# Kernel optimization log

Hardware: AMD Instinct MI355X
Metric: run time of the kernel (lower is better)

The kernel has to match this reference:

```python
import jax, jax.numpy as jnp
import numpy as np

EMBED_DIM = 1024
NUM_HEAD = 16
HEAD_DIM = EMBED_DIM // NUM_HEAD
SCALE = HEAD_DIM ** -0.5


def setup_inputs() -> dict:
    key = jax.random.key(0)
    ks = jax.random.split(key, 8)
    B, N, K, D = 2, 2048, 2048, EMBED_DIM
    s = D ** -0.5
    return {
        "x": jax.random.normal(ks[0], (B, N, D), jnp.float32),
        "ctx": jax.random.normal(ks[1], (B, K, D), jnp.float32),
        "Wq": jax.random.normal(ks[2], (D, D), jnp.float32) * s,
        "bq": jnp.zeros((D,), jnp.float32),
        "Wkv": jax.random.normal(ks[3], (D, 2 * D), jnp.float32) * s,
        "bkv": jnp.zeros((2 * D,), jnp.float32),
        "Wproj": jax.random.normal(ks[4], (D, D), jnp.float32) * s,
        "bproj": jnp.zeros((D,), jnp.float32),
    }


def reference(x, ctx, Wq, bq, Wkv, bkv, Wproj, bproj):
    B, N, D = x.shape
    K = ctx.shape[1]
    H, hd = NUM_HEAD, HEAD_DIM
    # Q projection -> [B, H, N, hd]
    q = (x @ Wq + bq).reshape(B, N, H, hd).transpose(0, 2, 1, 3)
    # KV projection -> k, v each [B, H, K, hd]
    kv = (ctx @ Wkv + bkv).reshape(B, K, 2, H, hd).transpose(2, 0, 3, 1, 4)
    k, v = kv[0], kv[1]
    # scaled dot-product attention with materialized scores [B, H, N, K]
    attn = jnp.einsum("bhnd,bhkd->bhnk", q * SCALE, k)
    attn = jax.nn.softmax(attn, axis=-1)
    out = jnp.einsum("bhnk,bhkd->bhnd", attn, v)
    out = out.transpose(0, 2, 1, 3).reshape(B, N, D)
    return out @ Wproj + bproj
```

## Files before the change

kernel.cpp:

```cpp
#include <hip/hip_runtime.h>
#include <hip/hip_bf16.h>

typedef __attribute__((ext_vector_type(8))) short bf16x8;
typedef __attribute__((ext_vector_type(4))) float f32x4;
typedef __attribute__((ext_vector_type(16))) float f32x16;
typedef unsigned short u16;
typedef unsigned int u32;

#define NUM_HEAD 16
#define HEAD_DIM 64
#define SEQ_N 2048
#define SEQ_K 2048
#define EMB 1024
#define MROWS 4096
static constexpr float ATTN_SCALE_LOG2E = 0.125f * 1.44269504f;

#if __has_builtin(__builtin_amdgcn_exp2f)
#define EXP2(x) __builtin_amdgcn_exp2f(x)
#else
#define EXP2(x) __expf(0.69314718056f * (x))
#endif

__device__ __forceinline__ u16 f2bf(float f) {
  __hip_bfloat16 h = __float2bfloat16(f);
  return *reinterpret_cast<u16*>(&h);
}

__device__ __forceinline__ u32 pack2(float lo, float hi) {
  __hip_bfloat162 h = __float22bfloat162_rn(make_float2(lo, hi));
  return *reinterpret_cast<u32*>(&h);
}

__device__ __forceinline__ void plswap(u32& a, u32& b) {
  auto r = __builtin_amdgcn_permlane32_swap(a, b, false, false);
  a = r[0]; b = r[1];
}

__device__ __forceinline__ void async16(const u16* g, u16* l) {
  __builtin_amdgcn_global_load_lds(
      (const __attribute__((address_space(1))) unsigned int*)g,
      (__attribute__((address_space(3))) unsigned int*)l, 16, 0, 0);
}

__global__ __launch_bounds__(256) void cvt2(const float* __restrict__ x,
                                            const float* __restrict__ ctx,
                                            u16* __restrict__ xb, u16* __restrict__ cb) {
  const int n4 = MROWS * EMB / 4;
  int gid = blockIdx.x * 256 + threadIdx.x;
  const float4* s; ushort4* d; int i;
  if (gid < n4) { s = (const float4*)x;   d = (ushort4*)xb; i = gid; }
  else          { s = (const float4*)ctx; d = (ushort4*)cb; i = gid - n4; }
  float4 v = s[i];
  ushort4 o;
  o.x = f2bf(v.x); o.y = f2bf(v.y); o.z = f2bf(v.z); o.w = f2bf(v.w);
  d[i] = o;
}

__global__ __launch_bounds__(256) void transpose_cvt4(
    const float* __restrict__ Wq, const float* __restrict__ Wkv,
    const float* __restrict__ Wproj,
    u16* __restrict__ Wqt, u16* __restrict__ Wkvt, u16* __restrict__ Wpt) {
  __shared__ float tile[32][33];
  const int z = blockIdx.z;
  const float* W; u16* Wt; int srcN, colbase;
  if (z == 0)      { W = Wq;    Wt = Wqt;                          srcN = 1024; colbase = 0; }
  else if (z == 1) { W = Wkv;   Wt = Wkvt;                         srcN = 2048; colbase = 0; }
  else if (z == 2) { W = Wkv;   Wt = Wkvt + (size_t)1024 * 1024;   srcN = 2048; colbase = 1024; }
  else             { W = Wproj; Wt = Wpt;                          srcN = 1024; colbase = 0; }
  int n0 = blockIdx.x * 32, k0 = blockIdx.y * 32;
  int tx = threadIdx.x & 31, ty = threadIdx.x >> 5;
  #pragma unroll
  for (int i = ty; i < 32; i += 8)
    tile[i][tx] = W[(size_t)(k0 + i) * srcN + colbase + n0 + tx];
  __syncthreads();
  #pragma unroll
  for (int i = ty; i < 32; i += 8)
    Wt[(size_t)(n0 + i) * 1024 + k0 + tx] = f2bf(tile[tx][i]);
}

__global__ __launch_bounds__(256, 3) void gemm_qkv(
    const u16* __restrict__ xb, const u16* __restrict__ cb,
    const u16* __restrict__ Wqt, const u16* __restrict__ Wkvt,
    const float* __restrict__ bq, const float* __restrict__ bkv,
    u16* __restrict__ Qb, u16* __restrict__ Kb, u16* __restrict__ Vtb)
{
  __shared__ alignas(16) u16 smem[(128 + 128) * 64];
  u16* As = smem;
  u16* Bs = smem + 128 * 64;
  const int tid = threadIdx.x;
  const bool isQ = (blockIdx.y < 8);
  const int n0 = (isQ ? blockIdx.y : blockIdx.y - 8) * 128;
  const int m0 = blockIdx.x * 128;
  const u16* A      = isQ ? xb : cb;
  const u16* Wt     = isQ ? Wqt : Wkvt;
  const float* bias = isQ ? bq : bkv;
  const int wave = tid >> 6, lane = tid & 63;
  const int wm = (wave >> 1) * 64, wn = (wave & 1) * 64;
  const int l15 = lane & 15, quad = lane >> 4;

  f32x4 acc[4][4];
  #pragma unroll
  for (int i = 0; i < 4; i++)
    #pragma unroll
    for (int j = 0; j < 4; j++)
      #pragma unroll
      for (int r = 0; r < 4; r++) acc[i][j][r] = 0.0f;

  const int srow = tid >> 3;
  const int scol = (tid & 7) * 8;
  const u16* ag = A + (size_t)(m0 + srow) * EMB + scol;
  const u16* bg = Wt + (size_t)(n0 + srow) * EMB + scol;
  const int ldsoff = tid * 8;

  for (int kt = 0; kt < EMB; kt += 64) {
    #pragma unroll
    for (int s = 0; s < 4; s++) {
      async16(ag + (size_t)(s * 32) * EMB + kt, &As[ldsoff + s * 2048]);
      async16(bg + (size_t)(s * 32) * EMB + kt, &Bs[ldsoff + s * 2048]);
    }
    __syncthreads();
    #pragma unroll
    for (int ks = 0; ks < 2; ks++) {
      bf16x8 af[4], bfr[4];
      #pragma unroll
      for (int i = 0; i < 4; i++)
        af[i]  = *(const bf16x8*)&As[(wm + i * 16 + l15) * 64 + ks * 32 + quad * 8];
      #pragma unroll
      for (int j = 0; j < 4; j++)
        bfr[j] = *(const bf16x8*)&Bs[(wn + j * 16 + l15) * 64 + ks * 32 + quad * 8];
      #pragma unroll
      for (int i = 0; i < 4; i++)
        #pragma unroll
        for (int j = 0; j < 4; j++)
          acc[i][j] = __builtin_amdgcn_mfma_f32_16x16x32_bf16(af[i], bfr[j], acc[i][j], 0, 0, 0);
    }
    __syncthreads();
  }

  const int h = ((n0 + wn) >> 6) & 15;
  if (isQ) {
    #pragma unroll
    for (int j = 0; j < 4; j++) {
      const int gc = n0 + wn + j * 16 + l15;
      const float bv = bias[gc];
      const int d = j * 16 + l15;
      #pragma unroll
      for (int i = 0; i < 4; i++) {
        #pragma unroll
        for (int r = 0; r < 4; r++) {
          const int gm = m0 + wm + i * 16 + quad * 4 + r;
          const int bb = gm >> 11, nn = gm & 2047;
          Qb[((size_t)(bb * NUM_HEAD + h) * SEQ_N + nn) * HEAD_DIM + d] =
              f2bf((acc[i][j][r] + bv) * ATTN_SCALE_LOG2E);
        }
      }
    }
  } else if ((n0 >> 10) == 0) {
    #pragma unroll
    for (int j = 0; j < 4; j++) {
      const int gc = n0 + wn + j * 16 + l15;
      const float bv = bias[gc];
      const int d = j * 16 + l15;
      #pragma unroll
      for (int i = 0; i < 4; i++) {
        #pragma unroll
        for (int r = 0; r < 4; r++) {
          const int gm = m0 + wm + i * 16 + quad * 4 + r;
          const int bb = gm >> 11, kk = gm & 2047;
          Kb[((size_t)(bb * NUM_HEAD + h) * SEQ_K + kk) * HEAD_DIM + d] =
              f2bf(acc[i][j][r] + bv);
        }
      }
    }
  } else {
    u16* wbuf = smem + wave * 1088;
    const int gm0 = m0 + wm;
    const int bb = gm0 >> 11;
    const int kk0 = gm0 & 2047;
    #pragma unroll
    for (int j = 0; j < 4; j++) {
      const int gc = n0 + wn + j * 16 + l15;
      const float bv = bias[gc];
      #pragma unroll
      for (int i = 0; i < 4; i++) {
        ushort4 pk;
        pk.x = f2bf(acc[i][j][0] + bv);
        pk.y = f2bf(acc[i][j][1] + bv);
        pk.z = f2bf(acc[i][j][2] + bv);
        pk.w = f2bf(acc[i][j][3] + bv);
        *(ushort4*)&wbuf[l15 * 68 + i * 16 + quad * 4] = pk;
      }
      #pragma unroll
      for (int it = 0; it < 2; it++) {
        const int dd = it * 8 + (lane >> 3);
        const int kp = (lane & 7) * 8;
        uint4 v = *(const uint4*)&wbuf[dd * 68 + kp];
        *(uint4*)(Vtb + ((size_t)(bb * NUM_HEAD + h) * HEAD_DIM + j * 16 + dd) * SEQ_K
                  + kk0 + kp) = v;
      }
    }
  }
}

__global__ __launch_bounds__(256) void gemm_proj(
    const u16* __restrict__ A, const u16* __restrict__ Wt,
    const float* __restrict__ bias, float* __restrict__ outF)
{
  __shared__ alignas(16) u16 smem[(64 + 128) * 64];
  u16* As = smem;
  u16* Bs = smem + 64 * 64;
  const int tid = threadIdx.x;
  const int n0 = blockIdx.y * 128, m0 = blockIdx.x * 64;
  const int wave = tid >> 6, lane = tid & 63;
  const int wm = (wave >> 1) * 32, wn = (wave & 1) * 64;
  const int l15 = lane & 15, quad = lane >> 4;

  f32x4 acc[2][4];
  #pragma unroll
  for (int i = 0; i < 2; i++)
    #pragma unroll
    for (int j = 0; j < 4; j++)
      #pragma unroll
      for (int r = 0; r < 4; r++) acc[i][j][r] = 0.0f;

  const int srow = tid >> 3;
  const int scol = (tid & 7) * 8;
  const u16* ag = A + (size_t)(m0 + srow) * EMB + scol;
  const u16* bg = Wt + (size_t)(n0 + srow) * EMB + scol;
  const int ldsoff = tid * 8;

  for (int kt = 0; kt < EMB; kt += 64) {
    async16(ag + kt, &As[ldsoff]);
    async16(ag + (size_t)32 * EMB + kt, &As[ldsoff + 2048]);
    #pragma unroll
    for (int s = 0; s < 4; s++)
      async16(bg + (size_t)(s * 32) * EMB + kt, &Bs[ldsoff + s * 2048]);
    __syncthreads();
    #pragma unroll
    for (int ks = 0; ks < 2; ks++) {
      bf16x8 af[2], bfr[4];
      #pragma unroll
      for (int i = 0; i < 2; i++)
        af[i]  = *(const bf16x8*)&As[(wm + i * 16 + l15) * 64 + ks * 32 + quad * 8];
      #pragma unroll
      for (int j = 0; j < 4; j++)
        bfr[j] = *(const bf16x8*)&Bs[(wn + j * 16 + l15) * 64 + ks * 32 + quad * 8];
      #pragma unroll
      for (int i = 0; i < 2; i++)
        #pragma unroll
        for (int j = 0; j < 4; j++)
          acc[i][j] = __builtin_amdgcn_mfma_f32_16x16x32_bf16(af[i], bfr[j], acc[i][j], 0, 0, 0);
    }
    __syncthreads();
  }

  #pragma unroll
  for (int i = 0; i < 2; i++) {
    #pragma unroll
    for (int j = 0; j < 4; j++) {
      const int gc = n0 + wn + j * 16 + l15;
      const float bv = bias[gc];
      #pragma unroll
      for (int r = 0; r < 4; r++) {
        const int gm = m0 + wm + i * 16 + quad * 4 + r;
        outF[(size_t)gm * EMB + gc] = acc[i][j][r] + bv;
      }
    }
  }
}

__global__ __launch_bounds__(256, 2) void attn_kernel(
    const u16* __restrict__ Qb, const u16* __restrict__ Kb,
    const u16* __restrict__ Vtb, u16* __restrict__ Ob)
{
  __shared__ alignas(16) u16 Ks[2][128 * 64];
  __shared__ alignas(16) u16 Vs[2][64 * 128];
  const int tid = threadIdx.x;
  const int bh = blockIdx.x;
  const int m0 = blockIdx.y * 128;
  const int wave = tid >> 6, lane = tid & 63;
  const int l31 = lane & 31, hi = lane >> 5;
  const int hi16 = hi * 16;
  const int swzK = (l31 & 7) << 4;
  const int swzV = (l31 & 15) << 4;
  const int rowb = m0 + wave * 32;

  bf16x8 bq[4];
  {
    const u16* qp = Qb + ((size_t)bh * SEQ_N + rowb + l31) * HEAD_DIM + hi * 8;
    #pragma unroll
    for (int db = 0; db < 4; db++) bq[db] = *(const bf16x8*)(qp + db * 16);
  }

  f32x16 o0, o1;
  #pragma unroll
  for (int r = 0; r < 16; r++) { o0[r] = 0.f; o1[r] = 0.f; }
  float l4[4] = {0.f, 0.f, 0.f, 0.f};

  const int krow0 = tid >> 3;
  const int ksg   = (tid & 7) ^ (krow0 & 7);
  const int vrow0 = tid >> 4;
  const int vsg   = (tid & 15) ^ vrow0;
  const u16* kg = Kb  + (size_t)bh * SEQ_K * HEAD_DIM;
  const u16* vg = Vtb + (size_t)bh * HEAD_DIM * SEQ_K;

#define STAGE(kt_, nb_) do {                                                   \
    _Pragma("unroll")                                                          \
    for (int s = 0; s < 4; s++) {                                              \
      async16(kg + (size_t)((kt_) + s * 32 + krow0) * HEAD_DIM + ksg * 8,      \
              &Ks[nb_][s * 2048 + tid * 8]);                                   \
      async16(vg + (size_t)(s * 16 + vrow0) * SEQ_K + (kt_) + vsg * 8,         \
              &Vs[nb_][s * 2048 + tid * 8]);                                   \
    }                                                                          \
  } while (0)

  STAGE(0, 0);
  __syncthreads();

  for (int kt = 0; kt < SEQ_K; kt += 128) {
    const int cur = (kt >> 7) & 1;
    if (kt + 128 < SEQ_K) STAGE(kt + 128, cur ^ 1);
    const char* KsB = (const char*)Ks[cur];
    const char* VsB = (const char*)Vs[cur];

    f32x16 sg[4];
    #pragma unroll
    for (int g = 0; g < 4; g++)
      #pragma unroll
      for (int r = 0; r < 16; r++) sg[g][r] = 0.f;
    __builtin_amdgcn_s_setprio(1);
    #pragma unroll
    for (int db = 0; db < 4; db++) {
      #pragma unroll
      for (int g = 0; g < 4; g++) {
        const bf16x8 ka = *(const bf16x8*)(
            KsB + (g * 32 + l31) * 128 + ((db * 32 + hi16) ^ swzK));
        sg[g] = __builtin_amdgcn_mfma_f32_32x32x16_bf16(ka, bq[db], sg[g], 0, 0, 0);
      }
    }
    __builtin_amdgcn_s_setprio(0);

    #pragma unroll
    for (int g = 0; g < 4; g++) {
      float p[16];
      #pragma unroll
      for (int r = 0; r < 16; r++) p[r] = EXP2(sg[g][r]);
      l4[g] += (((p[0] + p[1]) + (p[2] + p[3])) + ((p[4] + p[5]) + (p[6] + p[7])))
             + (((p[8] + p[9]) + (p[10] + p[11])) + ((p[12] + p[13]) + (p[14] + p[15])));
      u32 w0 = pack2(p[0],  p[1]),  w1 = pack2(p[2],  p[3]);
      u32 w2 = pack2(p[4],  p[5]),  w3 = pack2(p[6],  p[7]);
      u32 w4 = pack2(p[8],  p[9]),  w5 = pack2(p[10], p[11]);
      u32 w6 = pack2(p[12], p[13]), w7 = pack2(p[14], p[15]);
      plswap(w0, w2); plswap(w1, w3);
      plswap(w4, w6); plswap(w5, w7);
      union PU { u32 u[4]; bf16x8 v; } pa0, pa1;
      pa0.u[0] = w0; pa0.u[1] = w1; pa0.u[2] = w2; pa0.u[3] = w3;
      pa1.u[0] = w4; pa1.u[1] = w5; pa1.u[2] = w6; pa1.u[3] = w7;

      bf16x8 vb;
      __builtin_amdgcn_s_setprio(1);
      vb = *(const bf16x8*)(VsB + (l31)*256      + ((g * 64 + hi16)      ^ swzV));
      o0 = __builtin_amdgcn_mfma_f32_32x32x16_bf16(pa0.v, vb, o0, 0, 0, 0);
      vb = *(const bf16x8*)(VsB + (l31)*256      + ((g * 64 + 32 + hi16) ^ swzV));
      o0 = __builtin_amdgcn_mfma_f32_32x32x16_bf16(pa1.v, vb, o0, 0, 0, 0);
      vb = *(const bf16x8*)(VsB + (32 + l31)*256 + ((g * 64 + hi16)      ^ swzV));
      o1 = __builtin_amdgcn_mfma_f32_32x32x16_bf16(pa0.v, vb, o1, 0, 0, 0);
      vb = *(const bf16x8*)(VsB + (32 + l31)*256 + ((g * 64 + 32 + hi16) ^ swzV));
      o1 = __builtin_amdgcn_mfma_f32_32x32x16_bf16(pa1.v, vb, o1, 0, 0, 0);
      __builtin_amdgcn_s_setprio(0);
    }
    __syncthreads();
  }
#undef STAGE

  const float l_part = (l4[0] + l4[1]) + (l4[2] + l4[3]);
  const float lsum = l_part + __shfl_xor(l_part, 32, 64);
  const float inv = 1.0f / lsum;

  const int bb = bh >> 4, hh = bh & 15;
  #pragma unroll
  for (int r = 0; r < 16; r++) {
    const int qrow = (r & 3) + 8 * (r >> 2) + 4 * hi;
    const float invr = __shfl(inv, qrow, 64);
    const int gm = rowb + qrow;
    u16* op = Ob + ((size_t)bb * SEQ_N + gm) * EMB + hh * HEAD_DIM + l31;
    op[0]  = f2bf(o0[r] * invr);
    op[32] = f2bf(o1[r] * invr);
  }
}

extern "C" void kernel_launch(void* const* d_in, const int* in_sizes, int n_in,
                              void* d_out, int out_size, void* d_ws, size_t ws_size,
                              hipStream_t stream)
{
  const float* x     = (const float*)d_in[0];
  const float* ctx   = (const float*)d_in[1];
  const float* Wq    = (const float*)d_in[2];
  const float* bq    = (const float*)d_in[3];
  const float* Wkv   = (const float*)d_in[4];
  const float* bkv   = (const float*)d_in[5];
  const float* Wproj = (const float*)d_in[6];
  const float* bproj = (const float*)d_in[7];
  float* out = (float*)d_out;

  char* ws = (char*)d_ws;
  size_t off = 0;
  auto walloc = [&](size_t bytes) -> void* {
    void* p = ws + off;
    off += (bytes + 255) & ~(size_t)255;
    return p;
  };
  u16* xb   = (u16*)walloc((size_t)MROWS * EMB * 2);
  u16* cb   = (u16*)walloc((size_t)MROWS * EMB * 2);
  u16* Wqt  = (u16*)walloc((size_t)EMB * EMB * 2);
  u16* Wkvt = (u16*)walloc((size_t)2 * EMB * EMB * 2);
  u16* Wpt  = (u16*)walloc((size_t)EMB * EMB * 2);
  u16* Qb   = (u16*)walloc((size_t)MROWS * EMB * 2);
  u16* Kb   = (u16*)walloc((size_t)MROWS * EMB * 2);
  u16* Vtb  = (u16*)walloc((size_t)MROWS * EMB * 2);
  u16* Ob   = (u16*)walloc((size_t)MROWS * EMB * 2);

  cvt2<<<8192, 256, 0, stream>>>(x, ctx, xb, cb);
  transpose_cvt4<<<dim3(32, 32, 4), 256, 0, stream>>>(Wq, Wkv, Wproj, Wqt, Wkvt, Wpt);
  gemm_qkv<<<dim3(32, 24), 256, 0, stream>>>(xb, cb, Wqt, Wkvt, bq, bkv, Qb, Kb, Vtb);
  attn_kernel<<<dim3(32, 16), 256, 0, stream>>>(Qb, Kb, Vtb, Ob);
  gemm_proj<<<dim3(64, 8), 256, 0, stream>>>(Ob, Wpt, bproj, out);
}
```

Measured before the change: 201.7 us.

## Compute softmax denominator via MFMA with ones and interleave QK per group

The row sum of exponentials is now computed by extra MFMAs against a vector of bf16 ones, accumulated alongside the PV products, instead of 16 VALU adds per group. The final normalization uses a fast reciprocal per accumulator element and drops the cross-lane shuffle. The QK score computation is moved inside the per-group loop so only one score tile is live at a time, which reduces register pressure. In exchange this adds 50% more PV-stage MFMA work, and the denominator is summed from bf16-rounded probabilities.

```diff
diff --git a/kernel.cpp b/kernel.cpp
--- a/kernel.cpp
+++ b/kernel.cpp
@@ -19,6 +19,12 @@
 #define EXP2(x) __builtin_amdgcn_exp2f(x)
 #else
 #define EXP2(x) __expf(0.69314718056f * (x))
+#endif
+
+#if __has_builtin(__builtin_amdgcn_rcpf)
+#define RCP(x) __builtin_amdgcn_rcpf(x)
+#else
+#define RCP(x) (1.0f / (x))
 #endif
 
 __device__ __forceinline__ u16 f2bf(float f) {
@@ -292,10 +298,14 @@
     for (int db = 0; db < 4; db++) bq[db] = *(const bf16x8*)(qp + db * 16);
   }
 
-  f32x16 o0, o1;
-  #pragma unroll
-  for (int r = 0; r < 16; r++) { o0[r] = 0.f; o1[r] = 0.f; }
-  float l4[4] = {0.f, 0.f, 0.f, 0.f};
+  f32x16 o0, o1, od;
+  #pragma unroll
+  for (int r = 0; r < 16; r++) { o0[r] = 0.f; o1[r] = 0.f; od[r] = 0.f; }
+  f32x16 zc;
+  #pragma unroll
+  for (int r = 0; r < 16; r++) zc[r] = 0.f;
+  union { u32 u[4]; bf16x8 v; } ones;
+  ones.u[0] = ones.u[1] = ones.u[2] = ones.u[3] = 0x3F803F80u;
 
   const int krow0 = tid >> 3;
   const int ksg   = (tid & 7) ^ (krow0 & 7);
@@ -323,30 +333,21 @@
     const char* KsB = (const char*)Ks[cur];
     const char* VsB = (const char*)Vs[cur];
 
-    f32x16 sg[4];
-    #pragma unroll
-    for (int g = 0; g < 4; g++)
-      #pragma unroll
-      for (int r = 0; r < 16; r++) sg[g][r] = 0.f;
-    __builtin_amdgcn_s_setprio(1);
-    #pragma unroll
-    for (int db = 0; db < 4; db++) {
-      #pragma unroll
-      for (int g = 0; g < 4; g++) {
-        const bf16x8 ka = *(const bf16x8*)(
-            KsB + (g * 32 + l31) * 128 + ((db * 32 + hi16) ^ swzK));
-        sg[g] = __builtin_amdgcn_mfma_f32_32x32x16_bf16(ka, bq[db], sg[g], 0, 0, 0);
-      }
-    }
-    __builtin_amdgcn_s_setprio(0);
-
     #pragma unroll
     for (int g = 0; g < 4; g++) {
+      __builtin_amdgcn_s_setprio(1);
+      bf16x8 ka = *(const bf16x8*)(KsB + (g * 32 + l31) * 128 + (hi16 ^ swzK));
+      f32x16 s = __builtin_amdgcn_mfma_f32_32x32x16_bf16(ka, bq[0], zc, 0, 0, 0);
+      #pragma unroll
+      for (int db = 1; db < 4; db++) {
+        ka = *(const bf16x8*)(KsB + (g * 32 + l31) * 128 + ((db * 32 + hi16) ^ swzK));
+        s = __builtin_amdgcn_mfma_f32_32x32x16_bf16(ka, bq[db], s, 0, 0, 0);
+      }
+      __builtin_amdgcn_s_setprio(0);
+
       float p[16];
       #pragma unroll
-      for (int r = 0; r < 16; r++) p[r] = EXP2(sg[g][r]);
-      l4[g] += (((p[0] + p[1]) + (p[2] + p[3])) + ((p[4] + p[5]) + (p[6] + p[7])))
-             + (((p[8] + p[9]) + (p[10] + p[11])) + ((p[12] + p[13]) + (p[14] + p[15])));
+      for (int r = 0; r < 16; r++) p[r] = EXP2(s[r]);
       u32 w0 = pack2(p[0],  p[1]),  w1 = pack2(p[2],  p[3]);
       u32 w2 = pack2(p[4],  p[5]),  w3 = pack2(p[6],  p[7]);
       u32 w4 = pack2(p[8],  p[9]),  w5 = pack2(p[10], p[11]);
@@ -357,31 +358,28 @@
       pa0.u[0] = w0; pa0.u[1] = w1; pa0.u[2] = w2; pa0.u[3] = w3;
       pa1.u[0] = w4; pa1.u[1] = w5; pa1.u[2] = w6; pa1.u[3] = w7;
 
-      bf16x8 vb;
       __builtin_amdgcn_s_setprio(1);
-      vb = *(const bf16x8*)(VsB + (l31)*256      + ((g * 64 + hi16)      ^ swzV));
-      o0 = __builtin_amdgcn_mfma_f32_32x32x16_bf16(pa0.v, vb, o0, 0, 0, 0);
-      vb = *(const bf16x8*)(VsB + (l31)*256      + ((g * 64 + 32 + hi16) ^ swzV));
-      o0 = __builtin_amdgcn_mfma_f32_32x32x16_bf16(pa1.v, vb, o0, 0, 0, 0);
-      vb = *(const bf16x8*)(VsB + (32 + l31)*256 + ((g * 64 + hi16)      ^ swzV));
-      o1 = __builtin_amdgcn_mfma_f32_32x32x16_bf16(pa0.v, vb, o1, 0, 0, 0);
-      vb = *(const bf16x8*)(VsB + (32 + l31)*256 + ((g * 64 + 32 + hi16) ^ swzV));
-      o1 = __builtin_amdgcn_mfma_f32_32x32x16_bf16(pa1.v, vb, o1, 0, 0, 0);
+      bf16x8 vb00 = *(const bf16x8*)(VsB + (l31)*256      + ((g * 64 + hi16)      ^ swzV));
+      bf16x8 vb01 = *(const bf16x8*)(VsB + (l31)*256      + ((g * 64 + 32 + hi16) ^ swzV));
+      bf16x8 vb10 = *(const bf16x8*)(VsB + (32 + l31)*256 + ((g * 64 + hi16)      ^ swzV));
+      bf16x8 vb11 = *(const bf16x8*)(VsB + (32 + l31)*256 + ((g * 64 + 32 + hi16) ^ swzV));
+      o0 = __builtin_amdgcn_mfma_f32_32x32x16_bf16(pa0.v, vb00, o0, 0, 0, 0);
+      o1 = __builtin_amdgcn_mfma_f32_32x32x16_bf16(pa0.v, vb10, o1, 0, 0, 0);
+      od = __builtin_amdgcn_mfma_f32_32x32x16_bf16(pa0.v, ones.v, od, 0, 0, 0);
+      o0 = __builtin_amdgcn_mfma_f32_32x32x16_bf16(pa1.v, vb01, o0, 0, 0, 0);
+      o1 = __builtin_amdgcn_mfma_f32_32x32x16_bf16(pa1.v, vb11, o1, 0, 0, 0);
+      od = __builtin_amdgcn_mfma_f32_32x32x16_bf16(pa1.v, ones.v, od, 0, 0, 0);
       __builtin_amdgcn_s_setprio(0);
     }
     __syncthreads();
   }
 #undef STAGE
-
-  const float l_part = (l4[0] + l4[1]) + (l4[2] + l4[3]);
-  const float lsum = l_part + __shfl_xor(l_part, 32, 64);
-  const float inv = 1.0f / lsum;
 
   const int bb = bh >> 4, hh = bh & 15;
   #pragma unroll
   for (int r = 0; r < 16; r++) {
     const int qrow = (r & 3) + 8 * (r >> 2) + 4 * hi;
-    const float invr = __shfl(inv, qrow, 64);
+    const float invr = RCP(od[r]);
     const int gm = rowb + qrow;
     u16* op = Ob + ((size_t)bb * SEQ_N + gm) * EMB + hh * HEAD_DIM + l31;
     op[0]  = f2bf(o0[r] * invr);
```

After: 203.8 us. About the same (+1.0%).
